# Performance work log

Hardware: AMD Instinct MI355X
Metric: run time of the kernel (lower is better)

## Reference

```python
import jax, jax.numpy as jnp
import numpy as np

N, IN_DIM, HID, HEADS, OUT_DIM = 50000, 128, 64, 2, 40
E = 1_600_000
NEG_SLOPE = 0.2


def _glorot(key, shape):
    fan_in, fan_out = shape[0], shape[-1]
    lim = float(np.sqrt(6.0 / (fan_in + fan_out)))
    return jax.random.uniform(key, shape, jnp.float32, -lim, lim)


def setup_inputs() -> dict:
    key = jax.random.key(0)
    ks = jax.random.split(key, 20)
    x = jax.random.normal(ks[0], (N, IN_DIM), jnp.float32)
    edge_index = jax.random.randint(ks[1], (2, E), 0, N, jnp.int32)
    d = {"x": x, "edge_index": edge_index}
    # GAT layer 0: in=IN_DIM, out=HEADS*HID
    d["Wl0"] = _glorot(ks[2], (IN_DIM, HEADS * HID))
    d["bl0"] = jnp.zeros((HEADS * HID,), jnp.float32)
    d["Wr0"] = _glorot(ks[3], (IN_DIM, HEADS * HID))
    d["br0"] = jnp.zeros((HEADS * HID,), jnp.float32)
    d["al0"] = _glorot(ks[4], (HEADS, HID))
    d["ar0"] = _glorot(ks[5], (HEADS, HID))
    # GAT layer 1: in=HEADS*HID
    d["Wl1"] = _glorot(ks[6], (HEADS * HID, HEADS * HID))
    d["bl1"] = jnp.zeros((HEADS * HID,), jnp.float32)
    d["Wr1"] = _glorot(ks[7], (HEADS * HID, HEADS * HID))
    d["br1"] = jnp.zeros((HEADS * HID,), jnp.float32)
    d["al1"] = _glorot(ks[8], (HEADS, HID))
    d["ar1"] = _glorot(ks[9], (HEADS, HID))
    # post_mp: Linear(HEADS*HID, HID) -> Linear(HID, OUT_DIM)
    d["Wm1"] = _glorot(ks[10], (HEADS * HID, HID))
    d["bm1"] = jnp.zeros((HID,), jnp.float32)
    d["Wm2"] = _glorot(ks[11], (HID, OUT_DIM))
    d["bm2"] = jnp.zeros((OUT_DIM,), jnp.float32)
    return d


def _gat_layer(x, Wl, bl, Wr, br, al, ar, src, dst):
    # x: [N, F_in] -> [N, HEADS*HID]
    xl = (x @ Wl + bl).reshape(N, HEADS, HID)
    xr = (x @ Wr + br).reshape(N, HEADS, HID)
    alpha_l = jnp.einsum('nhc,hc->nh', xl, al)  # [N,H]
    alpha_r = jnp.einsum('nhc,hc->nh', xr, ar)  # [N,H]
    # per-edge attention logits: alpha_j (src) + alpha_i (dst)
    e = jax.nn.leaky_relu(alpha_l[src] + alpha_r[dst], NEG_SLOPE)  # [E,H]
    # segment softmax over incoming edges of each dst node
    m = jax.ops.segment_max(e, dst, num_segments=N)
    ex = jnp.exp(e - m[dst])
    s = jax.ops.segment_sum(ex, dst, num_segments=N)
    a = ex / (s[dst] + 1e-16)  # [E,H]
    # weighted scatter-sum of source features
    out = jax.ops.segment_sum(xl[src] * a[:, :, None], dst, num_segments=N)  # [N,H,C]
    return out.reshape(N, HEADS * HID)


def reference(x, edge_index, Wl0, bl0, Wr0, br0, al0, ar0,
              Wl1, bl1, Wr1, br1, al1, ar1, Wm1, bm1, Wm2, bm2):
    src, dst = edge_index[0], edge_index[1]
    h = jax.nn.relu(_gat_layer(x, Wl0, bl0, Wr0, br0, al0, ar0, src, dst))
    h = jax.nn.relu(_gat_layer(h, Wl1, bl1, Wr1, br1, al1, ar1, src, dst))
    h = (h @ Wm1 + bm1) @ Wm2 + bm2  # post_mp (dropout p=0.0)
    return jax.nn.log_softmax(h, axis=1)
```

## Files before the change

### kernel.cpp

```cpp
#include <hip/hip_runtime.h>
#include <hip/hip_fp16.h>
#include <math.h>

#define NN   50000
#define EE   1600000
#define FD   128
#define OUTD 40
#define NEG  0.2f
#define NB   196
#define ABLK 256
#define ACH  (EE/ABLK)
#define SLOTB 80
#define BMAX 9216
#define BPSZ (9*4*64*8)
#define SETUP_BLOCKS 2048

__device__ __forceinline__ float lrelu(float v) { return v > 0.f ? v : NEG * v; }

__device__ __forceinline__ int fenc(float f) { int b = __float_as_int(f); return b < 0 ? (b ^ 0x7FFFFFFF) : b; }
__device__ __forceinline__ float fdec(int v) { v = v < 0 ? (v ^ 0x7FFFFFFF) : v; return __int_as_float(v); }

__device__ __forceinline__ unsigned short f2bf(float f) {
  unsigned int u = __float_as_uint(f);
  unsigned int r = u + 0x7FFFu + ((u >> 16) & 1u);
  return (unsigned short)(r >> 16);
}

typedef short bf16x8 __attribute__((ext_vector_type(8)));
typedef float f32x4  __attribute__((ext_vector_type(4)));

__global__ __launch_bounds__(256) void k_setup(
    const float* __restrict__ X,
    const float* __restrict__ Wl0, const float* __restrict__ Wr0, const float* __restrict__ ar0,
    const float* __restrict__ br0,
    const float* __restrict__ Wl1, const float* __restrict__ Wr1, const float* __restrict__ ar1,
    const float* __restrict__ br1,
    const float* __restrict__ Wm1, const float* __restrict__ bm1,
    const float* __restrict__ Wm2, const float* __restrict__ bm2,
    unsigned short* __restrict__ XB,
    unsigned short* __restrict__ Bp0, unsigned short* __restrict__ Bp1,
    float* __restrict__ brd0, float* __restrict__ brd1,
    float* __restrict__ Wp, float* __restrict__ bp,
    int* __restrict__ mAL)
{
  int t = threadIdx.x;
  int bid = blockIdx.x;
  if (bid < 8) {
    for (int i = bid*256 + t; i < FD*OUTD; i += 8*256) {
      int k = i / OUTD, o = i % OUTD;
      float s = 0.f;
      for (int j = 0; j < 64; ++j) s += Wm1[k*64 + j] * Wm2[j*OUTD + o];
      Wp[i] = s;
    }
  } else if (bid == 8) {
    if (t < OUTD) {
      float s = bm2[t];
      for (int j = 0; j < 64; ++j) s += bm1[j] * Wm2[j*OUTD + t];
      bp[t] = s;
    }
    if (t >= 64 && t < 68) {
      int idx = t - 64, l = idx >> 1, h = idx & 1;
      const float* br = l ? br1 : br0;
      const float* ar = l ? ar1 : ar0;
      float s = 0.f;
      for (int c = 0; c < 64; ++c) s += br[h*64 + c] * ar[h*64 + c];
      (l ? brd1 : brd0)[h] = s;
    }
    if (t >= 96 && t < 100) mAL[t - 96] = 0x80000000;
  } else if (bid >= 16 && bid < 160) {
    bool l1 = (bid >= 88);
    const float* Wl = l1 ? Wl1 : Wl0;
    const float* Wr = l1 ? Wr1 : Wr0;
    const float* ar = l1 ? ar1 : ar0;
    unsigned short* Bp = l1 ? Bp1 : Bp0;
    int i = (bid - (l1 ? 88 : 16))*256 + t;
    if (i < BPSZ) {
      int j = i & 7, lane = (i >> 3) & 63, ks = (i >> 9) & 3, ct = i >> 11;
      int k = ks*32 + 8*(lane >> 4) + j;
      int c = lane & 15;
      float v = 0.f;
      if (ct < 8) v = Wl[k*FD + ct*16 + c];
      else if (c < 2) {
        for (int c2 = 0; c2 < 64; ++c2) v += Wr[k*FD + c*64 + c2] * ar[c*64 + c2];
      }
      Bp[i] = f2bf(v);
    }
  } else if (bid >= 160) {
    const int n4 = NN*FD/4;
    for (int i = (bid-160)*256 + t; i < n4; i += (gridDim.x-160)*256) {
      float4 v = ((const float4*)X)[i];
      ushort4 o;
      o.x = f2bf(v.x); o.y = f2bf(v.y); o.z = f2bf(v.z); o.w = f2bf(v.w);
      ((ushort4*)XB)[i] = o;
    }
  }
}

__global__ __launch_bounds__(256) void k_bplace(const int* __restrict__ src, const int* __restrict__ dst,
    int* __restrict__ cnt, unsigned int* __restrict__ pslot)
{
  __shared__ int lcur[NB];
  int t = threadIdx.x;
  int bid = blockIdx.x;
  if (t < NB) lcur[t] = 0;
  __syncthreads();
  int e0 = bid * ACH;
  size_t base = (size_t)bid * NB * SLOTB;
  for (int e = e0 + t; e < e0 + ACH; e += 256) {
    int d = dst[e];
    int b = d >> 8;
    int p = atomicAdd(&lcur[b], 1);
    pslot[base + (size_t)b*SLOTB + p] = (unsigned int)src[e] | ((unsigned int)(d & 255) << 16);
  }
  __syncthreads();
  if (t < NB) cnt[bid*NB + t] = lcur[t];
}

__global__ __launch_bounds__(256) void k_bfinal(const unsigned int* __restrict__ pslot,
    const int* __restrict__ cnt, int* __restrict__ row_off,
    unsigned short* __restrict__ csr16)
{
  __shared__ int scnt[256];
  __shared__ int soff[256];
  __shared__ unsigned int pairs[BMAX];
  __shared__ unsigned short stage[BMAX];
  __shared__ int hist[256];
  __shared__ int rel[256];
  int g = blockIdx.x;
  int t = threadIdx.x;
  int v = cnt[t*NB + g];
  scnt[t] = v;
  soff[t] = v;
  __syncthreads();
  #pragma unroll
  for (int off = 1; off < 256; off <<= 1) {
    int u = (t >= off) ? soff[t - off] : 0;
    __syncthreads();
    soff[t] += u;
    __syncthreads();
  }
  int cnt_g = soff[255];
  int mybase = soff[t] - v;
  {
    const unsigned int* sp = pslot + (size_t)t * NB * SLOTB + (size_t)g * SLOTB;
    for (int i = 0; i < v; ++i) pairs[mybase + i] = sp[i];
  }
  __syncthreads();
  hist[t] = 0;
  __syncthreads();
  for (int i = t; i < cnt_g; i += 256)
    atomicAdd(&hist[pairs[i] >> 16], 1);
  __syncthreads();
  int hv = hist[t];
  rel[t] = hv;
  __syncthreads();
  #pragma unroll
  for (int off = 1; off < 256; off <<= 1) {
    int u = (t >= off) ? rel[t - off] : 0;
    __syncthreads();
    rel[t] += u;
    __syncthreads();
  }
  int excl = rel[t] - hv;
  __syncthreads();
  rel[t] = excl;
  row_off[g*257 + t] = g*BMAX + excl;
  if (t == 0) row_off[g*257 + 256] = g*BMAX + cnt_g;
  hist[t] = 0;
  __syncthreads();
  for (int i = t; i < cnt_g; i += 256) {
    unsigned int p = pairs[i];
    int j = p >> 16;
    int l = atomicAdd(&hist[j], 1);
    stage[rel[j] + l] = (unsigned short)(p & 0xFFFF);
  }
  __syncthreads();
  size_t cbase = (size_t)g * BMAX;
  for (int i = t; i < cnt_g; i += 256) csr16[cbase + i] = stage[i];
}

__global__ __launch_bounds__(256) void k_gemm_mfma(
    const unsigned short* __restrict__ XB, const unsigned short* __restrict__ Bp,
    const float* __restrict__ bl, const float* __restrict__ al, const float* __restrict__ brd,
    __half* __restrict__ XLh, float* __restrict__ AL, float* __restrict__ AR,
    int* __restrict__ mAL)
{
  __shared__ unsigned short sB[BPSZ];
  __shared__ int smaxI[2];
  int t = threadIdx.x;
  if (t < 2) smaxI[t] = 0x80000000;
  {
    const uint4* s = (const uint4*)Bp;
    uint4* d = (uint4*)sB;
    #pragma unroll
    for (int i = 0; i < 9; ++i) d[t + i*256] = s[t + i*256];
  }
  __syncthreads();
  int w = t >> 6, l = t & 63;
  int c = l & 15, kg = l >> 4;
  int rowbase = blockIdx.x*64 + w*16;
  int arow = rowbase + c; if (arow > NN-1) arow = NN-1;
  f32x4 acc[9] = {};
  const bf16x8* sBf = (const bf16x8*)sB;
  #pragma unroll
  for (int ks = 0; ks < 4; ++ks) {
    bf16x8 afrag = *(const bf16x8*)(XB + (size_t)arow*FD + ks*32 + kg*8);
    #pragma unroll
    for (int ct = 0; ct < 9; ++ct)
      acc[ct] = __builtin_amdgcn_mfma_f32_16x16x32_bf16(afrag, sBf[(ct*4+ks)*64 + l], acc[ct], 0, 0, 0);
  }
  float pAL0[4] = {}, pAL1[4] = {};
  #pragma unroll
  for (int ct = 0; ct < 8; ++ct) {
    float bias = bl[ct*16 + c];
    float alv  = al[ct*16 + c];
    #pragma unroll
    for (int r = 0; r < 4; ++r) {
      int row = rowbase + kg*4 + r;
      float xv = acc[ct][r] + bias;
      if (row < NN) XLh[(size_t)row*FD + ct*16 + c] = __float2half(xv);
      if (ct < 4) pAL0[r] = fmaf(xv, alv, pAL0[r]);
      else        pAL1[r] = fmaf(xv, alv, pAL1[r]);
    }
  }
  if (c < 2) {
    float b = brd[c];
    #pragma unroll
    for (int r = 0; r < 4; ++r) {
      int row = rowbase + kg*4 + r;
      if (row < NN) AR[(size_t)row*2 + c] = acc[8][r] + b;
    }
  }
  float m0 = -INFINITY, m1 = -INFINITY;
  #pragma unroll
  for (int r = 0; r < 4; ++r) {
    float v0 = pAL0[r], v1 = pAL1[r];
    #pragma unroll
    for (int off = 1; off < 16; off <<= 1) { v0 += __shfl_xor(v0, off); v1 += __shfl_xor(v1, off); }
    int row = rowbase + kg*4 + r;
    if (c == 0 && row < NN) {
      AL[(size_t)row*2 + 0] = v0;
      AL[(size_t)row*2 + 1] = v1;
      m0 = fmaxf(m0, v0); m1 = fmaxf(m1, v1);
    }
  }
  if (c == 0) { atomicMax(&smaxI[0], fenc(m0)); atomicMax(&smaxI[1], fenc(m1)); }
  __syncthreads();
  if (t < 2) atomicMax(&mAL[t], smaxI[t]);
}

template<bool BF16OUT>
__global__ __launch_bounds__(256) void k_agg(
    const __half* __restrict__ XLh, const float* __restrict__ AL,
    const float* __restrict__ AR, const int* __restrict__ mAL,
    const int* __restrict__ row_off, const unsigned short* __restrict__ csr16,
    float* __restrict__ OUTf, unsigned short* __restrict__ OUTb)
{
  int node = blockIdx.x * 4 + (threadIdx.x >> 6);
  if (node >= NN) return;
  int lane = threadIdx.x & 63;
  int g = lane >> 4, l = lane & 15;
  bool h1 = (l & 8) != 0;
  float2 ar = ((const float2*)AR)[node];
  float m0 = lrelu(fdec(mAL[0]) + ar.x);
  float m1 = lrelu(fdec(mAL[1]) + ar.y);
  float ar_s = h1 ? ar.y : ar.x;
  float m_s  = h1 ? m1 : m0;
  int ro = node + (node >> 8);
  int beg = row_off[ro], end = row_off[ro + 1];
  float facc[8] = {};
  __half2 hacc[4];
  #pragma unroll
  for (int q = 0; q < 4; ++q) hacc[q] = __half2half2(__float2half(0.f));
  float s_acc = 0.f;
  int flushcnt = 0;
  if (beg < end) {
    int em1 = end - 1;
    int s0 = csr16[min(beg + g,      em1)];
    int s1 = csr16[min(beg + 4 + g,  em1)];
    int s2 = csr16[min(beg + 8 + g,  em1)];
    int s3 = csr16[min(beg + 12 + g, em1)];
    for (int i = beg; i < end; i += 16) {
      int c0 = s0, c1 = s1, c2 = s2, c3 = s3;
      bool v0 = (i + g) < end, v1 = (i + 4 + g) < end,
           v2 = (i + 8 + g) < end, v3 = (i + 12 + g) < end;
      int ni = i + 16;
      if (ni < end) {
        s0 = csr16[min(ni + g,      em1)];
        s1 = csr16[min(ni + 4 + g,  em1)];
        s2 = csr16[min(ni + 8 + g,  em1)];
        s3 = csr16[min(ni + 12 + g, em1)];
      }
      uint4 d0 = *(const uint4*)(XLh + (size_t)c0*FD + 8*l);
      uint4 d1 = *(const uint4*)(XLh + (size_t)c1*FD + 8*l);
      uint4 d2 = *(const uint4*)(XLh + (size_t)c2*FD + 8*l);
      uint4 d3 = *(const uint4*)(XLh + (size_t)c3*FD + 8*l);
      float2 a0 = ((const float2*)AL)[c0];
      float2 a1 = ((const float2*)AL)[c1];
      float2 a2 = ((const float2*)AL)[c2];
      float2 a3 = ((const float2*)AL)[c3];
      float w0 = __expf(lrelu((h1 ? a0.y : a0.x) + ar_s) - m_s);
      float w1 = __expf(lrelu((h1 ? a1.y : a1.x) + ar_s) - m_s);
      float w2 = __expf(lrelu((h1 ? a2.y : a2.x) + ar_s) - m_s);
      float w3 = __expf(lrelu((h1 ? a3.y : a3.x) + ar_s) - m_s);
      w0 = v0 ? w0 : 0.f; w1 = v1 ? w1 : 0.f;
      w2 = v2 ? w2 : 0.f; w3 = v3 ? w3 : 0.f;
      s_acc += (w0 + w1) + (w2 + w3);
      __half2 h0 = __half2half2(__float2half(w0));
      __half2 h1w = __half2half2(__float2half(w1));
      __half2 h2 = __half2half2(__float2half(w2));
      __half2 h3 = __half2half2(__float2half(w3));
      const __half2* f0 = (const __half2*)&d0;
      const __half2* f1 = (const __half2*)&d1;
      const __half2* f2 = (const __half2*)&d2;
      const __half2* f3 = (const __half2*)&d3;
      #pragma unroll
      for (int q = 0; q < 4; ++q) {
        hacc[q] = __hfma2(h0,  f0[q], hacc[q]);
        hacc[q] = __hfma2(h1w, f1[q], hacc[q]);
        hacc[q] = __hfma2(h2,  f2[q], hacc[q]);
        hacc[q] = __hfma2(h3,  f3[q], hacc[q]);
      }
      if (++flushcnt == 8) {
        flushcnt = 0;
        #pragma unroll
        for (int q = 0; q < 4; ++q) {
          float2 f = __half22float2(hacc[q]);
          facc[2*q] += f.x; facc[2*q+1] += f.y;
          hacc[q] = __half2half2(__float2half(0.f));
        }
      }
    }
    #pragma unroll
    for (int q = 0; q < 4; ++q) {
      float2 f = __half22float2(hacc[q]);
      facc[2*q] += f.x; facc[2*q+1] += f.y;
    }
  }
  #pragma unroll
  for (int off = 16; off < 64; off <<= 1) {
    s_acc += __shfl_xor(s_acc, off);
    #pragma unroll
    for (int q = 0; q < 8; ++q) facc[q] += __shfl_xor(facc[q], off);
  }
  if (g == 0) {
    float sinv = 1.f / (s_acc + 1e-16f);
    float o[8];
    #pragma unroll
    for (int q = 0; q < 8; ++q) o[q] = fmaxf(facc[q]*sinv, 0.f);
    if constexpr (BF16OUT) {
      unsigned short ob[8];
      #pragma unroll
      for (int q = 0; q < 8; ++q) ob[q] = f2bf(o[q]);
      *(uint4*)&OUTb[(size_t)node*FD + 8*l] = *(uint4*)ob;
    } else {
      float4 o0, o1;
      o0.x = o[0]; o0.y = o[1]; o0.z = o[2]; o0.w = o[3];
      o1.x = o[4]; o1.y = o[5]; o1.z = o[6]; o1.w = o[7];
      *(float4*)&OUTf[(size_t)node*FD + 8*l]     = o0;
      *(float4*)&OUTf[(size_t)node*FD + 8*l + 4] = o1;
    }
  }
}

__global__ __launch_bounds__(256) void k_post(
    const float* __restrict__ H, const float* __restrict__ Wp, const float* __restrict__ bp,
    float* __restrict__ out)
{
  __shared__ float sW[FD*OUTD];
  __shared__ float sB[OUTD];
  __shared__ float sX[64][FD+1];
  int t = threadIdx.x;
  for (int i = t; i < FD*OUTD; i += 256) sW[i] = Wp[i];
  if (t < OUTD) sB[t] = bp[t];
  int base = blockIdx.x * 64;
  int rows = NN - base; if (rows > 64) rows = 64;
  const float4* H4 = (const float4*)(H + (size_t)base * FD);
  int nf4 = rows * (FD/4);
  for (int i = t; i < nf4; i += 256) {
    float4 v = H4[i];
    int n = i >> 5, c = (i & 31) * 4;
    sX[n][c] = v.x; sX[n][c+1] = v.y; sX[n][c+2] = v.z; sX[n][c+3] = v.w;
  }
  __syncthreads();
  int n = t >> 2, cg = t & 3;
  int node = base + n;
  float acc[10];
  #pragma unroll
  for (int j = 0; j < 10; ++j) acc[j] = sB[cg*10 + j];
  #pragma unroll 4
  for (int k = 0; k < FD; ++k) {
    float xv = sX[n][k];
    const float* wrow = &sW[k*OUTD + cg*10];
    #pragma unroll
    for (int j = 0; j < 10; ++j) acc[j] = fmaf(xv, wrow[j], acc[j]);
  }
  float m = acc[0];
  #pragma unroll
  for (int j = 1; j < 10; ++j) m = fmaxf(m, acc[j]);
  m = fmaxf(m, __shfl_xor(m, 1));
  m = fmaxf(m, __shfl_xor(m, 2));
  float s = 0.f;
  #pragma unroll
  for (int j = 0; j < 10; ++j) s += __expf(acc[j] - m);
  s += __shfl_xor(s, 1);
  s += __shfl_xor(s, 2);
  float lg = m + __logf(s);
  if (node < NN) {
    #pragma unroll
    for (int j = 0; j < 10; ++j) out[(size_t)node*OUTD + cg*10 + j] = acc[j] - lg;
  }
}

extern "C" void kernel_launch(void* const* d_in, const int* in_sizes, int n_in,
                              void* d_out, int out_size, void* d_ws, size_t ws_size,
                              hipStream_t stream)
{
  const float* x   = (const float*)d_in[0];
  const int*   ei  = (const int*)d_in[1];
  const float* Wl0 = (const float*)d_in[2];
  const float* bl0 = (const float*)d_in[3];
  const float* Wr0 = (const float*)d_in[4];
  const float* br0 = (const float*)d_in[5];
  const float* al0 = (const float*)d_in[6];
  const float* ar0 = (const float*)d_in[7];
  const float* Wl1 = (const float*)d_in[8];
  const float* bl1 = (const float*)d_in[9];
  const float* Wr1 = (const float*)d_in[10];
  const float* br1 = (const float*)d_in[11];
  const float* al1 = (const float*)d_in[12];
  const float* ar1 = (const float*)d_in[13];
  const float* Wm1 = (const float*)d_in[14];
  const float* bm1 = (const float*)d_in[15];
  const float* Wm2 = (const float*)d_in[16];
  const float* bm2 = (const float*)d_in[17];
  const int* srcA = ei;
  const int* dstA = ei + EE;

  char* w = (char*)d_ws;
  __half* XLh    = (__half*)w;          w += (size_t)NN*FD*2;
  float* bufB    = (float*)w;           w += (size_t)NN*FD*4;
  unsigned short* XB = (unsigned short*)w; w += (size_t)NN*FD*2;
  float* AL      = (float*)w;  w += (size_t)NN*2*4;
  float* AR      = (float*)w;  w += (size_t)NN*2*4;
  float* brd0    = (float*)w;  w += 16;
  float* brd1    = (float*)w;  w += 16;
  float* Wp      = (float*)w;  w += FD*OUTD*4;
  float* bp      = (float*)w;  w += 64*4;
  int* mAL       = (int*)w;    w += 4*4;
  int* row_off   = (int*)w;    w += (size_t)(NB*257 + 1)*4 + 12;
  unsigned short* csr16 = (unsigned short*)w; w += (size_t)NB*BMAX*2;
  unsigned short* Bp0   = (unsigned short*)w; w += BPSZ*2;
  unsigned short* Bp1   = (unsigned short*)w; w += BPSZ*2;
  unsigned int* pslot = (unsigned int*)bufB;
  int* cnt = (int*)((char*)bufB + (size_t)ABLK*NB*SLOTB*4);

  k_setup<<<SETUP_BLOCKS, 256, 0, stream>>>(x, Wl0, Wr0, ar0, br0, Wl1, Wr1, ar1, br1,
                                            Wm1, bm1, Wm2, bm2, XB, Bp0, Bp1,
                                            brd0, brd1, Wp, bp, mAL);

  k_bplace<<<ABLK, 256, 0, stream>>>(srcA, dstA, cnt, pslot);
  k_bfinal<<<NB, 256, 0, stream>>>(pslot, cnt, row_off, csr16);

  k_gemm_mfma<<<(NN+63)/64, 256, 0, stream>>>(XB, Bp0, bl0, al0, brd0, XLh, AL, AR, mAL + 0);
  k_agg<true><<<(NN+3)/4, 256, 0, stream>>>(XLh, AL, AR, mAL + 0, row_off, csr16, nullptr, XB);
  k_gemm_mfma<<<(NN+63)/64, 256, 0, stream>>>(XB, Bp1, bl1, al1, brd1, XLh, AL, AR, mAL + 2);
  k_agg<false><<<(NN+3)/4, 256, 0, stream>>>(XLh, AL, AR, mAL + 2, row_off, csr16, bufB, nullptr);
  k_post<<<(NN+63)/64, 256, 0, stream>>>(bufB, Wp, bp, (float*)d_out);
}
```

Baseline: 208.1 us.

## Fuse edge bucketing into setup and CSR finalize into layer-0 GEMM launch

```diff
diff --git a/kernel.cpp b/kernel.cpp
--- a/kernel.cpp
+++ b/kernel.cpp
@@ -13,7 +13,7 @@
 #define SLOTB 80
 #define BMAX 9216
 #define BPSZ (9*4*64*8)
-#define SETUP_BLOCKS 2048
+#define SETUP_BLOCKS 2304
 
 __device__ __forceinline__ float lrelu(float v) { return v > 0.f ? v : NEG * v; }
 
@@ -31,6 +31,7 @@
 
 __global__ __launch_bounds__(256) void k_setup(
     const float* __restrict__ X,
+    const int* __restrict__ srcE, const int* __restrict__ dstE,
     const float* __restrict__ Wl0, const float* __restrict__ Wr0, const float* __restrict__ ar0,
     const float* __restrict__ br0,
     const float* __restrict__ Wl1, const float* __restrict__ Wr1, const float* __restrict__ ar1,
@@ -41,18 +42,34 @@
     unsigned short* __restrict__ Bp0, unsigned short* __restrict__ Bp1,
     float* __restrict__ brd0, float* __restrict__ brd1,
     float* __restrict__ Wp, float* __restrict__ bp,
-    int* __restrict__ mAL)
+    int* __restrict__ mAL,
+    int* __restrict__ cnt, unsigned int* __restrict__ pslot)
 {
+  __shared__ int lcur[NB];
   int t = threadIdx.x;
   int bid = blockIdx.x;
-  if (bid < 8) {
-    for (int i = bid*256 + t; i < FD*OUTD; i += 8*256) {
+  if (bid < 256) {
+    if (t < NB) lcur[t] = 0;
+    __syncthreads();
+    int e0 = bid * ACH;
+    size_t base = (size_t)bid * NB * SLOTB;
+    for (int e = e0 + t; e < e0 + ACH; e += 256) {
+      int d = dstE[e];
+      int b = d >> 8;
+      int p = atomicAdd(&lcur[b], 1);
+      pslot[base + (size_t)b*SLOTB + p] = (unsigned int)srcE[e] | ((unsigned int)(d & 255) << 16);
+    }
+    __syncthreads();
+    if (t < NB) cnt[bid*NB + t] = lcur[t];
+  } else if (bid < 264) {
+    int rb = bid - 256;
+    for (int i = rb*256 + t; i < FD*OUTD; i += 8*256) {
       int k = i / OUTD, o = i % OUTD;
       float s = 0.f;
       for (int j = 0; j < 64; ++j) s += Wm1[k*64 + j] * Wm2[j*OUTD + o];
       Wp[i] = s;
     }
-  } else if (bid == 8) {
+  } else if (bid == 264) {
     if (t < OUTD) {
       float s = bm2[t];
       for (int j = 0; j < 64; ++j) s += bm1[j] * Wm2[j*OUTD + t];
@@ -67,13 +84,13 @@
       (l ? brd1 : brd0)[h] = s;
     }
     if (t >= 96 && t < 100) mAL[t - 96] = 0x80000000;
-  } else if (bid >= 16 && bid < 160) {
-    bool l1 = (bid >= 88);
+  } else if (bid >= 272 && bid < 416) {
+    bool l1 = (bid >= 344);
     const float* Wl = l1 ? Wl1 : Wl0;
     const float* Wr = l1 ? Wr1 : Wr0;
     const float* ar = l1 ? ar1 : ar0;
     unsigned short* Bp = l1 ? Bp1 : Bp0;
-    int i = (bid - (l1 ? 88 : 16))*256 + t;
+    int i = (bid - (l1 ? 344 : 272))*256 + t;
     if (i < BPSZ) {
       int j = i & 7, lane = (i >> 3) & 63, ks = (i >> 9) & 3, ct = i >> 11;
       int k = ks*32 + 8*(lane >> 4) + j;
@@ -85,9 +102,9 @@
       }
       Bp[i] = f2bf(v);
     }
-  } else if (bid >= 160) {
+  } else if (bid >= 416) {
     const int n4 = NN*FD/4;
-    for (int i = (bid-160)*256 + t; i < n4; i += (gridDim.x-160)*256) {
+    for (int i = (bid-416)*256 + t; i < n4; i += (gridDim.x-416)*256) {
       float4 v = ((const float4*)X)[i];
       ushort4 o;
       o.x = f2bf(v.x); o.y = f2bf(v.y); o.z = f2bf(v.z); o.w = f2bf(v.w);
@@ -96,87 +113,138 @@
   }
 }
 
-__global__ __launch_bounds__(256) void k_bplace(const int* __restrict__ src, const int* __restrict__ dst,
-    int* __restrict__ cnt, unsigned int* __restrict__ pslot)
+#define SMEM_BYTES 59392
+__global__ __launch_bounds__(256) void k_bfgemm(
+    const unsigned int* __restrict__ pslot, const int* __restrict__ cnt,
+    int* __restrict__ row_off, unsigned short* __restrict__ csr16,
+    const unsigned short* __restrict__ XB, const unsigned short* __restrict__ Bp,
+    const float* __restrict__ bl, const float* __restrict__ al, const float* __restrict__ brd,
+    __half* __restrict__ XLh, float* __restrict__ AL, float* __restrict__ AR,
+    int* __restrict__ mAL)
 {
-  __shared__ int lcur[NB];
+  __shared__ char smem[SMEM_BYTES];
   int t = threadIdx.x;
   int bid = blockIdx.x;
-  if (t < NB) lcur[t] = 0;
-  __syncthreads();
-  int e0 = bid * ACH;
-  size_t base = (size_t)bid * NB * SLOTB;
-  for (int e = e0 + t; e < e0 + ACH; e += 256) {
-    int d = dst[e];
-    int b = d >> 8;
-    int p = atomicAdd(&lcur[b], 1);
-    pslot[base + (size_t)b*SLOTB + p] = (unsigned int)src[e] | ((unsigned int)(d & 255) << 16);
-  }
-  __syncthreads();
-  if (t < NB) cnt[bid*NB + t] = lcur[t];
-}
-
-__global__ __launch_bounds__(256) void k_bfinal(const unsigned int* __restrict__ pslot,
-    const int* __restrict__ cnt, int* __restrict__ row_off,
-    unsigned short* __restrict__ csr16)
-{
-  __shared__ int scnt[256];
-  __shared__ int soff[256];
-  __shared__ unsigned int pairs[BMAX];
-  __shared__ unsigned short stage[BMAX];
-  __shared__ int hist[256];
-  __shared__ int rel[256];
-  int g = blockIdx.x;
-  int t = threadIdx.x;
-  int v = cnt[t*NB + g];
-  scnt[t] = v;
-  soff[t] = v;
-  __syncthreads();
-  #pragma unroll
-  for (int off = 1; off < 256; off <<= 1) {
-    int u = (t >= off) ? soff[t - off] : 0;
-    __syncthreads();
-    soff[t] += u;
-    __syncthreads();
-  }
-  int cnt_g = soff[255];
-  int mybase = soff[t] - v;
-  {
-    const unsigned int* sp = pslot + (size_t)t * NB * SLOTB + (size_t)g * SLOTB;
-    for (int i = 0; i < v; ++i) pairs[mybase + i] = sp[i];
-  }
-  __syncthreads();
-  hist[t] = 0;
-  __syncthreads();
-  for (int i = t; i < cnt_g; i += 256)
-    atomicAdd(&hist[pairs[i] >> 16], 1);
-  __syncthreads();
-  int hv = hist[t];
-  rel[t] = hv;
-  __syncthreads();
-  #pragma unroll
-  for (int off = 1; off < 256; off <<= 1) {
-    int u = (t >= off) ? rel[t - off] : 0;
-    __syncthreads();
-    rel[t] += u;
-    __syncthreads();
-  }
-  int excl = rel[t] - hv;
-  __syncthreads();
-  rel[t] = excl;
-  row_off[g*257 + t] = g*BMAX + excl;
-  if (t == 0) row_off[g*257 + 256] = g*BMAX + cnt_g;
-  hist[t] = 0;
-  __syncthreads();
-  for (int i = t; i < cnt_g; i += 256) {
-    unsigned int p = pairs[i];
-    int j = p >> 16;
-    int l = atomicAdd(&hist[j], 1);
-    stage[rel[j] + l] = (unsigned short)(p & 0xFFFF);
-  }
-  __syncthreads();
-  size_t cbase = (size_t)g * BMAX;
-  for (int i = t; i < cnt_g; i += 256) csr16[cbase + i] = stage[i];
+  if (bid < NB) {
+    int* scnt = (int*)smem;
+    int* soff = (int*)(smem + 1024);
+    unsigned int* pairs = (unsigned int*)(smem + 2048);
+    unsigned short* stage = (unsigned short*)(smem + 38912);
+    int* hist = (int*)(smem + 57344);
+    int* rel  = (int*)(smem + 58368);
+    int g = bid;
+    int v = cnt[t*NB + g];
+    scnt[t] = v;
+    soff[t] = v;
+    __syncthreads();
+    #pragma unroll
+    for (int off = 1; off < 256; off <<= 1) {
+      int u = (t >= off) ? soff[t - off] : 0;
+      __syncthreads();
+      soff[t] += u;
+      __syncthreads();
+    }
+    int cnt_g = soff[255];
+    int mybase = soff[t] - v;
+    {
+      const unsigned int* sp = pslot + (size_t)t * NB * SLOTB + (size_t)g * SLOTB;
+      for (int i = 0; i < v; ++i) pairs[mybase + i] = sp[i];
+    }
+    __syncthreads();
+    hist[t] = 0;
+    __syncthreads();
+    for (int i = t; i < cnt_g; i += 256)
+      atomicAdd(&hist[pairs[i] >> 16], 1);
+    __syncthreads();
+    int hv = hist[t];
+    rel[t] = hv;
+    __syncthreads();
+    #pragma unroll
+    for (int off = 1; off < 256; off <<= 1) {
+      int u = (t >= off) ? rel[t - off] : 0;
+      __syncthreads();
+      rel[t] += u;
+      __syncthreads();
+    }
+    int excl = rel[t] - hv;
+    __syncthreads();
+    rel[t] = excl;
+    row_off[g*257 + t] = g*BMAX + excl;
+    if (t == 0) row_off[g*257 + 256] = g*BMAX + cnt_g;
+    hist[t] = 0;
+    __syncthreads();
+    for (int i = t; i < cnt_g; i += 256) {
+      unsigned int p = pairs[i];
+      int j = p >> 16;
+      int l = atomicAdd(&hist[j], 1);
+      stage[rel[j] + l] = (unsigned short)(p & 0xFFFF);
+    }
+    __syncthreads();
+    size_t cbase = (size_t)g * BMAX;
+    for (int i = t; i < cnt_g; i += 256) csr16[cbase + i] = stage[i];
+  } else {
+    unsigned short* sB = (unsigned short*)smem;
+    int* smaxI = (int*)(smem + 36864);
+    if (t < 2) smaxI[t] = 0x80000000;
+    {
+      const uint4* s = (const uint4*)Bp;
+      uint4* d = (uint4*)sB;
+      #pragma unroll
+      for (int i = 0; i < 9; ++i) d[t + i*256] = s[t + i*256];
+    }
+    __syncthreads();
+    int w = t >> 6, l = t & 63;
+    int c = l & 15, kg = l >> 4;
+    int rowbase = (bid - NB)*64 + w*16;
+    int arow = rowbase + c; if (arow > NN-1) arow = NN-1;
+    f32x4 acc[9] = {};
+    const bf16x8* sBf = (const bf16x8*)sB;
+    #pragma unroll
+    for (int ks = 0; ks < 4; ++ks) {
+      bf16x8 afrag = *(const bf16x8*)(XB + (size_t)arow*FD + ks*32 + kg*8);
+      #pragma unroll
+      for (int ct = 0; ct < 9; ++ct)
+        acc[ct] = __builtin_amdgcn_mfma_f32_16x16x32_bf16(afrag, sBf[(ct*4+ks)*64 + l], acc[ct], 0, 0, 0);
+    }
+    float pAL0[4] = {}, pAL1[4] = {};
+    #pragma unroll
+    for (int ct = 0; ct < 8; ++ct) {
+      float bias = bl[ct*16 + c];
+      float alv  = al[ct*16 + c];
+      #pragma unroll
+      for (int r = 0; r < 4; ++r) {
+        int row = rowbase + kg*4 + r;
+        float xv = acc[ct][r] + bias;
+        if (row < NN) XLh[(size_t)row*FD + ct*16 + c] = __float2half(xv);
+        if (ct < 4) pAL0[r] = fmaf(xv, alv, pAL0[r]);
+        else        pAL1[r] = fmaf(xv, alv, pAL1[r]);
+      }
+    }
+    if (c < 2) {
+      float b = brd[c];
+      #pragma unroll
+      for (int r = 0; r < 4; ++r) {
+        int row = rowbase + kg*4 + r;
+        if (row < NN) AR[(size_t)row*2 + c] = acc[8][r] + b;
+      }
+    }
+    float m0 = -INFINITY, m1 = -INFINITY;
+    #pragma unroll
+    for (int r = 0; r < 4; ++r) {
+      float v0 = pAL0[r], v1 = pAL1[r];
+      #pragma unroll
+      for (int off = 1; off < 16; off <<= 1) { v0 += __shfl_xor(v0, off); v1 += __shfl_xor(v1, off); }
+      int row = rowbase + kg*4 + r;
+      if (c == 0 && row < NN) {
+        AL[(size_t)row*2 + 0] = v0;
+        AL[(size_t)row*2 + 1] = v1;
+        m0 = fmaxf(m0, v0); m1 = fmaxf(m1, v1);
+      }
+    }
+    if (c == 0) { atomicMax(&smaxI[0], fenc(m0)); atomicMax(&smaxI[1], fenc(m1)); }
+    __syncthreads();
+    if (t < 2) atomicMax(&mAL[t], smaxI[t]);
+  }
 }
 
 __global__ __launch_bounds__(256) void k_gemm_mfma(
@@ -455,14 +523,13 @@
   unsigned int* pslot = (unsigned int*)bufB;
   int* cnt = (int*)((char*)bufB + (size_t)ABLK*NB*SLOTB*4);
 
-  k_setup<<<SETUP_BLOCKS, 256, 0, stream>>>(x, Wl0, Wr0, ar0, br0, Wl1, Wr1, ar1, br1,
+  k_setup<<<SETUP_BLOCKS, 256, 0, stream>>>(x, srcA, dstA,
+                                            Wl0, Wr0, ar0, br0, Wl1, Wr1, ar1, br1,
                                             Wm1, bm1, Wm2, bm2, XB, Bp0, Bp1,
-                                            brd0, brd1, Wp, bp, mAL);
-
-  k_bplace<<<ABLK, 256, 0, stream>>>(srcA, dstA, cnt, pslot);
-  k_bfinal<<<NB, 256, 0, stream>>>(pslot, cnt, row_off, csr16);
-
-  k_gemm_mfma<<<(NN+63)/64, 256, 0, stream>>>(XB, Bp0, bl0, al0, brd0, XLh, AL, AR, mAL + 0);
+                                            brd0, brd1, Wp, bp, mAL, cnt, pslot);
+
+  k_bfgemm<<<NB + (NN+63)/64, 256, 0, stream>>>(pslot, cnt, row_off, csr16,
+                                                XB, Bp0, bl0, al0, brd0, XLh, AL, AR, mAL + 0);
   k_agg<true><<<(NN+3)/4, 256, 0, stream>>>(XLh, AL, AR, mAL + 0, row_off, csr16, nullptr, XB);
   k_gemm_mfma<<<(NN+63)/64, 256, 0, stream>>>(XB, Bp1, bl1, al1, brd1, XLh, AL, AR, mAL + 2);
   k_agg<false><<<(NN+3)/4, 256, 0, stream>>>(XLh, AL, AR, mAL + 2, row_off, csr16, bufB, nullptr);
```

Result: faster. 190.2 us (-8.6%).
